# Performance work log

Hardware: AMD Instinct MI355X
Metric: run time of the kernel (lower is better)

## Reference

```python
import jax, jax.numpy as jnp
import numpy as np

DIM = 1024
HID = 512
N_EXPERTS = 16
TOP_K = 4


def setup_inputs() -> dict:
    key = jax.random.key(0)
    ks = jax.random.split(key, 8)
    s = 0.02
    x = jax.random.normal(ks[0], (2, 1024, DIM), dtype=jnp.float32)
    gate_w = jax.random.normal(ks[1], (N_EXPERTS, DIM), dtype=jnp.float32) * s
    # stacked expert weights (nn.Linear stores [out, in]; we keep [E, out, in])
    w1 = jax.random.normal(ks[2], (N_EXPERTS, HID, DIM), dtype=jnp.float32) * s
    w3 = jax.random.normal(ks[3], (N_EXPERTS, HID, DIM), dtype=jnp.float32) * s
    w2 = jax.random.normal(ks[4], (N_EXPERTS, DIM, HID), dtype=jnp.float32) * s
    sw1 = jax.random.normal(ks[5], (HID, DIM), dtype=jnp.float32) * s
    sw3 = jax.random.normal(ks[6], (HID, DIM), dtype=jnp.float32) * s
    sw2 = jax.random.normal(ks[7], (DIM, HID), dtype=jnp.float32) * s
    return {"x": x, "gate_w": gate_w, "w1": w1, "w3": w3, "w2": w2,
            "sw1": sw1, "sw3": sw3, "sw2": sw2}


def reference(x, gate_w, w1, w3, w2, sw1, sw3, sw2):
    bsz, seq_len, dim = x.shape
    xf = x.reshape(-1, dim)                              # [T, d]
    T = xf.shape[0]

    # router: softmax -> top-k -> renormalize
    probs = jax.nn.softmax(xf @ gate_w.T, axis=-1)       # [T, E]
    top_w, top_idx = jax.lax.top_k(probs, TOP_K)         # [T, K]
    top_w = top_w / jnp.sum(top_w, axis=-1, keepdims=True)

    # combine weights as dense [T, E] (zero for unselected experts);
    # weighted dense per-expert compute is mathematically identical to the
    # gather/scatter loop since unselected experts get weight 0.
    rows = jnp.arange(T)[:, None]
    combine = jnp.zeros((T, N_EXPERTS), dtype=xf.dtype).at[rows, top_idx].set(top_w)

    h1 = jnp.einsum('td,ehd->teh', xf, w1)               # [T, E, h]
    h3 = jnp.einsum('td,ehd->teh', xf, w3)
    act = jax.nn.silu(h1) * h3
    eout = jnp.einsum('teh,edh->ted', act, w2)           # [T, E, d]
    moe_out = jnp.einsum('ted,te->td', eout, combine)    # [T, d]

    shared = (jax.nn.silu(xf @ sw1.T) * (xf @ sw3.T)) @ sw2.T
    return (moe_out + shared).reshape(bsz, seq_len, dim)
```

## Files before the change

kernel.cpp:

```cpp
#include <hip/hip_runtime.h>

#define DIM   1024
#define HID   512
#define NEXP  16
#define TOPK  4
#define SLOTS 5
#define PITCH 72
#define TPE   16

typedef unsigned short u16;
typedef unsigned int   u32;
typedef short bf16x8 __attribute__((ext_vector_type(8)));
typedef float f32x4  __attribute__((ext_vector_type(4)));

__device__ __forceinline__ float bf2f(u16 u) {
    union { u32 i; float f; } v; v.i = ((u32)u) << 16; return v.f;
}
__device__ __forceinline__ u16 f2bf(float f) {
    union { float f; u32 i; } v; v.f = f;
    u32 lsb = (v.i >> 16) & 1u;
    v.i += 0x7fffu + lsb;
    return (u16)(v.i >> 16);
}
__device__ __forceinline__ uint4 pack8(float4 a, float4 b) {
    uint4 r;
    r.x = (u32)f2bf(a.x) | ((u32)f2bf(a.y) << 16);
    r.y = (u32)f2bf(a.z) | ((u32)f2bf(a.w) << 16);
    r.z = (u32)f2bf(b.x) | ((u32)f2bf(b.y) << 16);
    r.w = (u32)f2bf(b.z) | ((u32)f2bf(b.w) << 16);
    return r;
}

#define CW ((size_t)NEXP * HID * DIM / 8)
#define CS ((size_t)HID * DIM / 8)
#define SEG_B0 (CW)
#define SEG_B1 (SEG_B0 + CS)
#define SEG_B2 (SEG_B1 + CW)
#define SEG_B3 (SEG_B2 + CS)
#define SEG_B4 (SEG_B3 + CW)
#define SEG_B5 (SEG_B4 + CS)

__global__ __launch_bounds__(256) void moe_prep(
    const float* __restrict__ x,    const float* __restrict__ gate,
    const float* __restrict__ w1,   const float* __restrict__ w3,
    const float* __restrict__ w2,   const float* __restrict__ sw1,
    const float* __restrict__ sw3,  const float* __restrict__ sw2,
    u16* __restrict__ dst,
    int* __restrict__ counts, u32* __restrict__ pairs,
    float* __restrict__ wslot, int T)
{
    const int blk = blockIdx.x;
    const int tid = threadIdx.x;
    if (blk >= T) {
        const size_t base = (size_t)(blk - T) * 512 + tid;
        const size_t totC = SEG_B5 + ((size_t)T << 7);
#pragma unroll
        for (int h = 0; h < 2; ++h) {
            const size_t c = base + (size_t)h * 256;
            if (c >= totC) break;
            const float* src; size_t loc;
            if      (c < SEG_B0) { src = w1;  loc = c; }
            else if (c < SEG_B1) { src = sw1; loc = c - SEG_B0; }
            else if (c < SEG_B2) { src = w3;  loc = c - SEG_B1; }
            else if (c < SEG_B3) { src = sw3; loc = c - SEG_B2; }
            else if (c < SEG_B4) { src = w2;  loc = c - SEG_B3; }
            else if (c < SEG_B5) { src = sw2; loc = c - SEG_B4; }
            else                 { src = x;   loc = c - SEG_B5; }
            float4 a = ((const float4*)src)[loc * 2];
            float4 b = ((const float4*)src)[loc * 2 + 1];
            ((uint4*)dst)[c] = pack8(a, b);
        }
        return;
    }
    const int t    = blk;
    const int lane = tid & 63;
    const int wv   = tid >> 6;
    const float* xrow = x + (size_t)t * DIM;
    float xr[16];
#pragma unroll
    for (int j = 0; j < 16; ++j) xr[j] = xrow[lane + 64 * j];

    __shared__ float slog[NEXP];
#pragma unroll
    for (int i = 0; i < 4; ++i) {
        const int e = wv * 4 + i;
        const float* g = gate + (size_t)e * DIM;
        float s = 0.f;
#pragma unroll
        for (int j = 0; j < 16; ++j) s += xr[j] * g[lane + 64 * j];
#pragma unroll
        for (int off = 32; off > 0; off >>= 1) s += __shfl_xor(s, off);
        if (lane == 0) slog[e] = s;
    }
    __syncthreads();
    if (wv != 0) return;

    float v[NEXP];
#pragma unroll
    for (int e = 0; e < NEXP; ++e) v[e] = slog[e];
    int idx[TOPK]; float lv[TOPK];
#pragma unroll
    for (int r = 0; r < TOPK; ++r) {
        int be = 0; float bv = v[0];
        for (int e = 1; e < NEXP; ++e) { if (v[e] > bv) { bv = v[e]; be = e; } }
        idx[r] = be; lv[r] = bv; v[be] = -3.0e38f;
    }
    float wk[TOPK]; float wsum = 0.f;
#pragma unroll
    for (int r = 0; r < TOPK; ++r) { wk[r] = __expf(lv[r] - lv[0]); wsum += wk[r]; }
#pragma unroll
    for (int r = 0; r < TOPK; ++r) wk[r] /= wsum;

    if (lane < TOPK) {
        int e = idx[lane];
        int slot = atomicAdd(&counts[e], 1);
        if (slot < T) pairs[(size_t)e * T + slot] = ((u32)t << 3) | (u32)lane;
        wslot[t * SLOTS + lane] = wk[lane];
    } else if (lane == TOPK) {
        pairs[(size_t)NEXP * T + t] = ((u32)t << 3) | 4u;
        wslot[t * SLOTS + 4] = 1.0f;
    }
}

__global__ __launch_bounds__(256) void moe_gemm1(
    const u16* __restrict__ xb,
    const u16* __restrict__ w1c, const u16* __restrict__ w3c,
    const u32* __restrict__ pairs, const int* __restrict__ counts,
    u16* __restrict__ act, int T)
{
    const int e   = blockIdx.y >> 4;
    const int r0  = (blockIdx.y & (TPE - 1)) << 7;
    const int cnt = (e == NEXP) ? T : min(max(counts[e], 0), T);
    if (r0 >= cnt) return;
    const int nv = min(128, cnt - r0);
    const int n0 = blockIdx.x * 64;

    const u16* W1 = w1c + (size_t)e * HID * DIM;
    const u16* W3 = w3c + (size_t)e * HID * DIM;

    __shared__ __align__(16) u16 sA [128 * PITCH];
    __shared__ __align__(16) u16 sB1[ 64 * PITCH];
    __shared__ __align__(16) u16 sB3[ 64 * PITCH];
    __shared__ u32 sEnt[128];

    const int tid = threadIdx.x;
    if (tid < 128) {
        u32 ent = (tid < nv) ? pairs[(size_t)e * T + r0 + tid] : 0u;
        u32 tk = ent >> 3, sl = ent & 7u;
        if (tk >= (u32)T) tk = 0;
        if (sl >= SLOTS)  sl = 0;
        sEnt[tid] = (tk << 3) | sl;
    }
    __syncthreads();

    const int ar = tid >> 1;
    const int ac = (tid & 1) * 32;
    const u16* xrow = xb + (size_t)(sEnt[ar] >> 3) * DIM;
    const int br = tid >> 2;
    const int bc = (tid & 3) * 16;
    const u16* b1row = W1 + (size_t)(n0 + br) * DIM;
    const u16* b3row = W3 + (size_t)(n0 + br) * DIM;

    const int wv   = tid >> 6;
    const int lane = tid & 63;
    const int l15  = lane & 15;
    const int kq   = (lane >> 4) * 8;
    const int m0   = wv * 32;

    f32x4 acc1[2][4], acc3[2][4];
#pragma unroll
    for (int i = 0; i < 2; ++i)
#pragma unroll
        for (int j = 0; j < 4; ++j) { acc1[i][j] = (f32x4){0,0,0,0}; acc3[i][j] = (f32x4){0,0,0,0}; }

    for (int kt = 0; kt < DIM; kt += 64) {
        __syncthreads();
        *(uint4*)&sA [ar*PITCH + ac]      = *(const uint4*)&xrow [kt + ac];
        *(uint4*)&sA [ar*PITCH + ac +  8] = *(const uint4*)&xrow [kt + ac +  8];
        *(uint4*)&sA [ar*PITCH + ac + 16] = *(const uint4*)&xrow [kt + ac + 16];
        *(uint4*)&sA [ar*PITCH + ac + 24] = *(const uint4*)&xrow [kt + ac + 24];
        *(uint4*)&sB1[br*PITCH + bc]      = *(const uint4*)&b1row[kt + bc];
        *(uint4*)&sB1[br*PITCH + bc +  8] = *(const uint4*)&b1row[kt + bc + 8];
        *(uint4*)&sB3[br*PITCH + bc]      = *(const uint4*)&b3row[kt + bc];
        *(uint4*)&sB3[br*PITCH + bc +  8] = *(const uint4*)&b3row[kt + bc + 8];
        __syncthreads();
#pragma unroll
        for (int ks = 0; ks < 64; ks += 32) {
            bf16x8 a0 = *(const bf16x8*)&sA[(m0      + l15)*PITCH + ks + kq];
            bf16x8 a1 = *(const bf16x8*)&sA[(m0 + 16 + l15)*PITCH + ks + kq];
#pragma unroll
            for (int nt = 0; nt < 4; ++nt) {
                bf16x8 b1 = *(const bf16x8*)&sB1[(nt*16 + l15)*PITCH + ks + kq];
                bf16x8 b3 = *(const bf16x8*)&sB3[(nt*16 + l15)*PITCH + ks + kq];
                acc1[0][nt] = __builtin_amdgcn_mfma_f32_16x16x32_bf16(a0, b1, acc1[0][nt], 0, 0, 0);
                acc1[1][nt] = __builtin_amdgcn_mfma_f32_16x16x32_bf16(a1, b1, acc1[1][nt], 0, 0, 0);
                acc3[0][nt] = __builtin_amdgcn_mfma_f32_16x16x32_bf16(a0, b3, acc3[0][nt], 0, 0, 0);
                acc3[1][nt] = __builtin_amdgcn_mfma_f32_16x16x32_bf16(a1, b3, acc3[1][nt], 0, 0, 0);
            }
        }
    }
#pragma unroll
    for (int mf = 0; mf < 2; ++mf)
#pragma unroll
    for (int nt = 0; nt < 4; ++nt)
#pragma unroll
    for (int r = 0; r < 4; ++r) {
        int ml = m0 + mf*16 + (lane >> 4)*4 + r;
        if (ml < nv) {
            float h1 = acc1[mf][nt][r], h3 = acc3[mf][nt][r];
            float a = (h1 / (1.f + __expf(-h1))) * h3;
            u32 ent = sEnt[ml];
            size_t sidx = (size_t)(ent >> 3) * SLOTS + (ent & 7u);
            act[sidx * HID + n0 + nt*16 + l15] = f2bf(a);
        }
    }
}

__global__ __launch_bounds__(256) void moe_gemm2(
    const u16* __restrict__ act, const u16* __restrict__ w2c,
    const u32* __restrict__ pairs, const float* __restrict__ wslot,
    const int* __restrict__ counts,
    u16* __restrict__ eout, float* __restrict__ out, int useEout, int T)
{
    const int e   = blockIdx.y >> 4;
    const int r0  = (blockIdx.y & (TPE - 1)) << 7;
    const int cnt = (e == NEXP) ? T : min(max(counts[e], 0), T);
    if (r0 >= cnt) return;
    const int nv = min(128, cnt - r0);
    const int n0 = blockIdx.x * 128;

    const u16* W2 = w2c + (size_t)e * DIM * HID;

    __shared__ __align__(16) u16 sA[128 * PITCH];
    __shared__ __align__(16) u16 sB[128 * PITCH];
    __shared__ u32 sEnt[128];

    const int tid = threadIdx.x;
    if (tid < 128) {
        u32 ent = (tid < nv) ? pairs[(size_t)e * T + r0 + tid] : 0u;
        u32 tk = ent >> 3, sl = ent & 7u;
        if (tk >= (u32)T) tk = 0;
        if (sl >= SLOTS)  sl = 0;
        sEnt[tid] = (tk << 3) | sl;
    }
    __syncthreads();

    const int ar = tid >> 1;
    const int ac = (tid & 1) * 32;
    const u32 entA = sEnt[ar];
    const u16* arow = act + ((size_t)(entA >> 3) * SLOTS + (entA & 7u)) * HID;
    const u16* brow = W2 + (size_t)(n0 + ar) * HID;

    const int wv   = tid >> 6;
    const int lane = tid & 63;
    const int l15  = lane & 15;
    const int kq   = (lane >> 4) * 8;
    const int m0   = (wv & 1) * 64;
    const int nc0  = (wv >> 1) * 64;

    f32x4 acc[4][4];
#pragma unroll
    for (int i = 0; i < 4; ++i)
#pragma unroll
        for (int j = 0; j < 4; ++j) acc[i][j] = (f32x4){0,0,0,0};

    for (int kt = 0; kt < HID; kt += 64) {
        __syncthreads();
        *(uint4*)&sA[ar*PITCH + ac]      = *(const uint4*)&arow[kt + ac];
        *(uint4*)&sA[ar*PITCH + ac +  8] = *(const uint4*)&arow[kt + ac +  8];
        *(uint4*)&sA[ar*PITCH + ac + 16] = *(const uint4*)&arow[kt + ac + 16];
        *(uint4*)&sA[ar*PITCH + ac + 24] = *(const uint4*)&arow[kt + ac + 24];
        *(uint4*)&sB[ar*PITCH + ac]      = *(const uint4*)&brow[kt + ac];
        *(uint4*)&sB[ar*PITCH + ac +  8] = *(const uint4*)&brow[kt + ac +  8];
        *(uint4*)&sB[ar*PITCH + ac + 16] = *(const uint4*)&brow[kt + ac + 16];
        *(uint4*)&sB[ar*PITCH + ac + 24] = *(const uint4*)&brow[kt + ac + 24];
        __syncthreads();
#pragma unroll
        for (int ks = 0; ks < 64; ks += 32) {
            bf16x8 af[4], bf[4];
#pragma unroll
            for (int mf = 0; mf < 4; ++mf)
                af[mf] = *(const bf16x8*)&sA[(m0 + mf*16 + l15)*PITCH + ks + kq];
#pragma unroll
            for (int nf = 0; nf < 4; ++nf)
                bf[nf] = *(const bf16x8*)&sB[(nc0 + nf*16 + l15)*PITCH + ks + kq];
#pragma unroll
            for (int mf = 0; mf < 4; ++mf)
#pragma unroll
                for (int nf = 0; nf < 4; ++nf)
                    acc[mf][nf] = __builtin_amdgcn_mfma_f32_16x16x32_bf16(af[mf], bf[nf], acc[mf][nf], 0, 0, 0);
        }
    }
#pragma unroll
    for (int mf = 0; mf < 4; ++mf)
#pragma unroll
    for (int nf = 0; nf < 4; ++nf)
#pragma unroll
    for (int r = 0; r < 4; ++r) {
        int ml = m0 + mf*16 + (lane >> 4)*4 + r;
        if (ml < nv) {
            u32 ent = sEnt[ml];
            u32 tk = ent >> 3;
            float cw = wslot[tk * SLOTS + (ent & 7u)];
            int col = n0 + nc0 + nf*16 + l15;
            float v = cw * acc[mf][nf][r];
            if (useEout) {
                size_t sidx = (size_t)tk * SLOTS + (ent & 7u);
                eout[sidx * DIM + col] = f2bf(v);
            } else {
                atomicAdd(&out[(size_t)tk * DIM + col], v);
            }
        }
    }
}

__global__ __launch_bounds__(256) void moe_combine(
    const u16* __restrict__ eout, float* __restrict__ out, int n4)
{
    int i = blockIdx.x * 256 + threadIdx.x;
    if (i >= n4) return;
    int o4 = i * 4;
    int t = o4 >> 10;
    int col = o4 & 1023;
    float a0 = 0.f, a1 = 0.f, a2 = 0.f, a3 = 0.f;
#pragma unroll
    for (int s = 0; s < SLOTS; ++s) {
        const u16* row = eout + ((size_t)t * SLOTS + s) * DIM + col;
        ushort4 u = *(const ushort4*)row;
        a0 += bf2f(u.x); a1 += bf2f(u.y); a2 += bf2f(u.z); a3 += bf2f(u.w);
    }
    float4* op = (float4*)(out + (size_t)t * DIM + col);
    *op = (float4){a0, a1, a2, a3};
}

extern "C" void kernel_launch(void* const* d_in, const int* in_sizes, int n_in,
                              void* d_out, int out_size, void* d_ws, size_t ws_size,
                              hipStream_t stream)
{
    (void)n_in; (void)out_size;
    const float* x    = (const float*)d_in[0];
    const float* gate = (const float*)d_in[1];
    const float* w1   = (const float*)d_in[2];
    const float* w3   = (const float*)d_in[3];
    const float* w2   = (const float*)d_in[4];
    const float* sw1  = (const float*)d_in[5];
    const float* sw3  = (const float*)d_in[6];
    const float* sw2  = (const float*)d_in[7];
    float* out = (float*)d_out;
    const int T = in_sizes[0] / DIM;

    char* w = (char*)d_ws;
    int*  counts = (int*)(w);
    size_t off = 4096;
    u32*   pairs = (u32*)(w + off);  off += (size_t)(NEXP + 1) * T * 4;
    float* wslot = (float*)(w + off); off += (size_t)T * SLOTS * 4;
    off = (off + 255) & ~(size_t)255;
    u16*   actb  = (u16*)(w + off);  off += (size_t)T * SLOTS * HID * 2;
    off = (off + 255) & ~(size_t)255;
    u16*   cvtb  = (u16*)(w + off);
    const size_t xChunks = (size_t)T * DIM / 8;
    const size_t cvtChunks = SEG_B5 + xChunks;
    off += cvtChunks * 8 * 2;
    off = (off + 255) & ~(size_t)255;
    u16*   eoutb = (u16*)(w + off);
    const size_t needEout = off + (size_t)T * SLOTS * DIM * 2;

    u16* W1c = cvtb;
    u16* W3c = cvtb + SEG_B1 * 8;
    u16* W2c = cvtb + SEG_B3 * 8;
    u16* xb  = cvtb + SEG_B5 * 8;

    const int useEout = (ws_size >= needEout) ? 1 : 0;

    hipMemsetAsync(w, 0, 256, stream);
    if (!useEout)
        hipMemsetAsync(out, 0, (size_t)T * DIM * sizeof(float), stream);

    const int nCvt = (int)((cvtChunks + 511) / 512);
    moe_prep<<<T + nCvt, 256, 0, stream>>>(
        x, gate, w1, w3, w2, sw1, sw3, sw2, cvtb, counts, pairs, wslot, T);

    moe_gemm1<<<dim3(HID / 64, (NEXP + 1) * TPE), 256, 0, stream>>>(
        xb, W1c, W3c, pairs, counts, actb, T);
    moe_gemm2<<<dim3(DIM / 128, (NEXP + 1) * TPE), 256, 0, stream>>>(
        actb, W2c, pairs, wslot, counts, eoutb, out, useEout, T);
    if (useEout)
        moe_combine<<<(T * DIM / 4 + 255) / 256, 256, 0, stream>>>(
            eoutb, out, T * DIM / 4);
}
```

Baseline: 266.9 us.

## Fuse fp32-to-bf16 conversion into GEMM tile loads and swizzle block order

Removes the separate bulk conversion pass that turned all expert weights and x into bf16 in a workspace. The GEMM kernels now read fp32 weights and activations directly and pack them to bf16 while staging tiles into shared memory. The grids become 1D with a block-index swizzle so that blocks sharing a weight tile or row tile run close together. In exchange each GEMM tile load moves twice the bytes from global memory, and weight tiles reused by several row tiles get converted more than once.

New measurement: 381.5 us. +43.0%, slower.

```diff
diff --git a/kernel.cpp b/kernel.cpp
--- a/kernel.cpp
+++ b/kernel.cpp
@@ -31,48 +31,13 @@
     return r;
 }
 
-#define CW ((size_t)NEXP * HID * DIM / 8)
-#define CS ((size_t)HID * DIM / 8)
-#define SEG_B0 (CW)
-#define SEG_B1 (SEG_B0 + CS)
-#define SEG_B2 (SEG_B1 + CW)
-#define SEG_B3 (SEG_B2 + CS)
-#define SEG_B4 (SEG_B3 + CW)
-#define SEG_B5 (SEG_B4 + CS)
-
-__global__ __launch_bounds__(256) void moe_prep(
-    const float* __restrict__ x,    const float* __restrict__ gate,
-    const float* __restrict__ w1,   const float* __restrict__ w3,
-    const float* __restrict__ w2,   const float* __restrict__ sw1,
-    const float* __restrict__ sw3,  const float* __restrict__ sw2,
-    u16* __restrict__ dst,
+__global__ __launch_bounds__(256) void moe_router(
+    const float* __restrict__ x, const float* __restrict__ gate,
     int* __restrict__ counts, u32* __restrict__ pairs,
     float* __restrict__ wslot, int T)
 {
-    const int blk = blockIdx.x;
-    const int tid = threadIdx.x;
-    if (blk >= T) {
-        const size_t base = (size_t)(blk - T) * 512 + tid;
-        const size_t totC = SEG_B5 + ((size_t)T << 7);
-#pragma unroll
-        for (int h = 0; h < 2; ++h) {
-            const size_t c = base + (size_t)h * 256;
-            if (c >= totC) break;
-            const float* src; size_t loc;
-            if      (c < SEG_B0) { src = w1;  loc = c; }
-            else if (c < SEG_B1) { src = sw1; loc = c - SEG_B0; }
-            else if (c < SEG_B2) { src = w3;  loc = c - SEG_B1; }
-            else if (c < SEG_B3) { src = sw3; loc = c - SEG_B2; }
-            else if (c < SEG_B4) { src = w2;  loc = c - SEG_B3; }
-            else if (c < SEG_B5) { src = sw2; loc = c - SEG_B4; }
-            else                 { src = x;   loc = c - SEG_B5; }
-            float4 a = ((const float4*)src)[loc * 2];
-            float4 b = ((const float4*)src)[loc * 2 + 1];
-            ((uint4*)dst)[c] = pack8(a, b);
-        }
-        return;
-    }
-    const int t    = blk;
+    const int t    = blockIdx.x;
+    const int tid  = threadIdx.x;
     const int lane = tid & 63;
     const int wv   = tid >> 6;
     const float* xrow = x + (size_t)t * DIM;
@@ -122,21 +87,26 @@
     }
 }
 
+#define NB1 ((HID / 64) * (NEXP + 1) * TPE)
 __global__ __launch_bounds__(256) void moe_gemm1(
-    const u16* __restrict__ xb,
-    const u16* __restrict__ w1c, const u16* __restrict__ w3c,
+    const float* __restrict__ x,
+    const float* __restrict__ w1,  const float* __restrict__ w3,
+    const float* __restrict__ sw1, const float* __restrict__ sw3,
     const u32* __restrict__ pairs, const int* __restrict__ counts,
     u16* __restrict__ act, int T)
 {
-    const int e   = blockIdx.y >> 4;
-    const int r0  = (blockIdx.y & (TPE - 1)) << 7;
+    const int lin = blockIdx.x;
+    const int swz = (lin & 7) * (NB1 / 8) + (lin >> 3);
+    const int ytile = swz >> 3;
+    const int n0    = (swz & 7) * 64;
+    const int e   = ytile >> 4;
+    const int r0  = (ytile & (TPE - 1)) << 7;
     const int cnt = (e == NEXP) ? T : min(max(counts[e], 0), T);
     if (r0 >= cnt) return;
     const int nv = min(128, cnt - r0);
-    const int n0 = blockIdx.x * 64;
-
-    const u16* W1 = w1c + (size_t)e * HID * DIM;
-    const u16* W3 = w3c + (size_t)e * HID * DIM;
+
+    const float* W1 = (e == NEXP) ? sw1 : w1 + (size_t)e * HID * DIM;
+    const float* W3 = (e == NEXP) ? sw3 : w3 + (size_t)e * HID * DIM;
 
     __shared__ __align__(16) u16 sA [128 * PITCH];
     __shared__ __align__(16) u16 sB1[ 64 * PITCH];
@@ -155,11 +125,11 @@
 
     const int ar = tid >> 1;
     const int ac = (tid & 1) * 32;
-    const u16* xrow = xb + (size_t)(sEnt[ar] >> 3) * DIM;
+    const float* xrow = x + (size_t)(sEnt[ar] >> 3) * DIM;
     const int br = tid >> 2;
     const int bc = (tid & 3) * 16;
-    const u16* b1row = W1 + (size_t)(n0 + br) * DIM;
-    const u16* b3row = W3 + (size_t)(n0 + br) * DIM;
+    const float* b1row = W1 + (size_t)(n0 + br) * DIM;
+    const float* b3row = W3 + (size_t)(n0 + br) * DIM;
 
     const int wv   = tid >> 6;
     const int lane = tid & 63;
@@ -175,14 +145,23 @@
 
     for (int kt = 0; kt < DIM; kt += 64) {
         __syncthreads();
-        *(uint4*)&sA [ar*PITCH + ac]      = *(const uint4*)&xrow [kt + ac];
-        *(uint4*)&sA [ar*PITCH + ac +  8] = *(const uint4*)&xrow [kt + ac +  8];
-        *(uint4*)&sA [ar*PITCH + ac + 16] = *(const uint4*)&xrow [kt + ac + 16];
-        *(uint4*)&sA [ar*PITCH + ac + 24] = *(const uint4*)&xrow [kt + ac + 24];
-        *(uint4*)&sB1[br*PITCH + bc]      = *(const uint4*)&b1row[kt + bc];
-        *(uint4*)&sB1[br*PITCH + bc +  8] = *(const uint4*)&b1row[kt + bc + 8];
-        *(uint4*)&sB3[br*PITCH + bc]      = *(const uint4*)&b3row[kt + bc];
-        *(uint4*)&sB3[br*PITCH + bc +  8] = *(const uint4*)&b3row[kt + bc + 8];
+        {
+            const float4* ap = (const float4*)(xrow + kt + ac);
+            float4 a0 = ap[0], a1 = ap[1], a2 = ap[2], a3 = ap[3];
+            float4 a4 = ap[4], a5 = ap[5], a6 = ap[6], a7 = ap[7];
+            const float4* q1 = (const float4*)(b1row + kt + bc);
+            float4 q0 = q1[0], q1v = q1[1], q2 = q1[2], q3 = q1[3];
+            const float4* p3 = (const float4*)(b3row + kt + bc);
+            float4 r0v = p3[0], r1v = p3[1], r2v = p3[2], r3v = p3[3];
+            *(uint4*)&sA [ar*PITCH + ac]      = pack8(a0, a1);
+            *(uint4*)&sA [ar*PITCH + ac +  8] = pack8(a2, a3);
+            *(uint4*)&sA [ar*PITCH + ac + 16] = pack8(a4, a5);
+            *(uint4*)&sA [ar*PITCH + ac + 24] = pack8(a6, a7);
+            *(uint4*)&sB1[br*PITCH + bc]      = pack8(q0, q1v);
+            *(uint4*)&sB1[br*PITCH + bc +  8] = pack8(q2, q3);
+            *(uint4*)&sB3[br*PITCH + bc]      = pack8(r0v, r1v);
+            *(uint4*)&sB3[br*PITCH + bc +  8] = pack8(r2v, r3v);
+        }
         __syncthreads();
 #pragma unroll
         for (int ks = 0; ks < 64; ks += 32) {
@@ -216,20 +195,25 @@
     }
 }
 
+#define NB2 ((DIM / 128) * (NEXP + 1) * TPE)
 __global__ __launch_bounds__(256) void moe_gemm2(
-    const u16* __restrict__ act, const u16* __restrict__ w2c,
+    const u16* __restrict__ act,
+    const float* __restrict__ w2, const float* __restrict__ sw2,
     const u32* __restrict__ pairs, const float* __restrict__ wslot,
     const int* __restrict__ counts,
     u16* __restrict__ eout, float* __restrict__ out, int useEout, int T)
 {
-    const int e   = blockIdx.y >> 4;
-    const int r0  = (blockIdx.y & (TPE - 1)) << 7;
+    const int lin = blockIdx.x;
+    const int swz = (lin & 7) * (NB2 / 8) + (lin >> 3);
+    const int ytile = swz >> 3;
+    const int n0    = (swz & 7) * 128;
+    const int e   = ytile >> 4;
+    const int r0  = (ytile & (TPE - 1)) << 7;
     const int cnt = (e == NEXP) ? T : min(max(counts[e], 0), T);
     if (r0 >= cnt) return;
     const int nv = min(128, cnt - r0);
-    const int n0 = blockIdx.x * 128;
-
-    const u16* W2 = w2c + (size_t)e * DIM * HID;
+
+    const float* W2 = (e == NEXP) ? sw2 : w2 + (size_t)e * DIM * HID;
 
     __shared__ __align__(16) u16 sA[128 * PITCH];
     __shared__ __align__(16) u16 sB[128 * PITCH];
@@ -248,8 +232,8 @@
     const int ar = tid >> 1;
     const int ac = (tid & 1) * 32;
     const u32 entA = sEnt[ar];
-    const u16* arow = act + ((size_t)(entA >> 3) * SLOTS + (entA & 7u)) * HID;
-    const u16* brow = W2 + (size_t)(n0 + ar) * HID;
+    const u16*  arow = act + ((size_t)(entA >> 3) * SLOTS + (entA & 7u)) * HID;
+    const float* brow = W2 + (size_t)(n0 + ar) * HID;
 
     const int wv   = tid >> 6;
     const int lane = tid & 63;
@@ -266,14 +250,19 @@
 
     for (int kt = 0; kt < HID; kt += 64) {
         __syncthreads();
-        *(uint4*)&sA[ar*PITCH + ac]      = *(const uint4*)&arow[kt + ac];
-        *(uint4*)&sA[ar*PITCH + ac +  8] = *(const uint4*)&arow[kt + ac +  8];
-        *(uint4*)&sA[ar*PITCH + ac + 16] = *(const uint4*)&arow[kt + ac + 16];
-        *(uint4*)&sA[ar*PITCH + ac + 24] = *(const uint4*)&arow[kt + ac + 24];
-        *(uint4*)&sB[ar*PITCH + ac]      = *(const uint4*)&brow[kt + ac];
-        *(uint4*)&sB[ar*PITCH + ac +  8] = *(const uint4*)&brow[kt + ac +  8];
-        *(uint4*)&sB[ar*PITCH + ac + 16] = *(const uint4*)&brow[kt + ac + 16];
-        *(uint4*)&sB[ar*PITCH + ac + 24] = *(const uint4*)&brow[kt + ac + 24];
+        {
+            *(uint4*)&sA[ar*PITCH + ac]      = *(const uint4*)&arow[kt + ac];
+            *(uint4*)&sA[ar*PITCH + ac +  8] = *(const uint4*)&arow[kt + ac +  8];
+            *(uint4*)&sA[ar*PITCH + ac + 16] = *(const uint4*)&arow[kt + ac + 16];
+            *(uint4*)&sA[ar*PITCH + ac + 24] = *(const uint4*)&arow[kt + ac + 24];
+            const float4* bp = (const float4*)(brow + kt + ac);
+            float4 b0 = bp[0], b1 = bp[1], b2 = bp[2], b3 = bp[3];
+            float4 b4 = bp[4], b5 = bp[5], b6 = bp[6], b7 = bp[7];
+            *(uint4*)&sB[ar*PITCH + ac]      = pack8(b0, b1);
+            *(uint4*)&sB[ar*PITCH + ac +  8] = pack8(b2, b3);
+            *(uint4*)&sB[ar*PITCH + ac + 16] = pack8(b4, b5);
+            *(uint4*)&sB[ar*PITCH + ac + 24] = pack8(b6, b7);
+        }
         __syncthreads();
 #pragma unroll
         for (int ks = 0; ks < 64; ks += 32) {
@@ -357,18 +346,8 @@
     off = (off + 255) & ~(size_t)255;
     u16*   actb  = (u16*)(w + off);  off += (size_t)T * SLOTS * HID * 2;
     off = (off + 255) & ~(size_t)255;
-    u16*   cvtb  = (u16*)(w + off);
-    const size_t xChunks = (size_t)T * DIM / 8;
-    const size_t cvtChunks = SEG_B5 + xChunks;
-    off += cvtChunks * 8 * 2;
-    off = (off + 255) & ~(size_t)255;
     u16*   eoutb = (u16*)(w + off);
     const size_t needEout = off + (size_t)T * SLOTS * DIM * 2;
-
-    u16* W1c = cvtb;
-    u16* W3c = cvtb + SEG_B1 * 8;
-    u16* W2c = cvtb + SEG_B3 * 8;
-    u16* xb  = cvtb + SEG_B5 * 8;
 
     const int useEout = (ws_size >= needEout) ? 1 : 0;
 
@@ -376,14 +355,12 @@
     if (!useEout)
         hipMemsetAsync(out, 0, (size_t)T * DIM * sizeof(float), stream);
 
-    const int nCvt = (int)((cvtChunks + 511) / 512);
-    moe_prep<<<T + nCvt, 256, 0, stream>>>(
-        x, gate, w1, w3, w2, sw1, sw3, sw2, cvtb, counts, pairs, wslot, T);
-
-    moe_gemm1<<<dim3(HID / 64, (NEXP + 1) * TPE), 256, 0, stream>>>(
-        xb, W1c, W3c, pairs, counts, actb, T);
-    moe_gemm2<<<dim3(DIM / 128, (NEXP + 1) * TPE), 256, 0, stream>>>(
-        actb, W2c, pairs, wslot, counts, eoutb, out, useEout, T);
+    moe_router<<<T, 256, 0, stream>>>(x, gate, counts, pairs, wslot, T);
+
+    moe_gemm1<<<NB1, 256, 0, stream>>>(
+        x, w1, w3, sw1, sw3, pairs, counts, actb, T);
+    moe_gemm2<<<NB2, 256, 0, stream>>>(
+        actb, w2, sw2, pairs, wslot, counts, eoutb, out, useEout, T);
     if (useEout)
         moe_combine<<<(T * DIM / 4 + 255) / 256, 256, 0, stream>>>(
             eoutb, out, T * DIM / 4);
```

## Enlarge GEMM tiles: 128x128 dual-B tile in gemm1, 256x128 tile in gemm2

Applied to the files above, without the earlier changes.

The gate/up GEMM now computes a 128-token by 128-hidden tile per block, with each wave holding a 64x64 sub-tile for both W1 and W3. The down-projection GEMM now covers 256 rows by 128 output columns, and each wave computes a 64x128 sub-tile. Larger tiles raise MFMA work per LDS fragment load and cut redundant global loads of weights and activations. The cost is more accumulator registers (acc1/acc3 at 4x4 each, acc at 4x8) and more LDS per block, so occupancy may drop, and there are fewer blocks to spread across CUs.

Result: slower. 403.3 us (+51.1%).

```diff
diff --git a/kernel.cpp b/kernel.cpp
--- a/kernel.cpp
+++ b/kernel.cpp
@@ -7,6 +7,7 @@
 #define SLOTS 5
 #define PITCH 72
 #define TPE   16
+#define TPE2  8
 
 typedef unsigned short u16;
 typedef unsigned int   u32;
@@ -128,19 +129,20 @@
     const u32* __restrict__ pairs, const int* __restrict__ counts,
     u16* __restrict__ act, int T)
 {
-    const int e   = blockIdx.y >> 4;
-    const int r0  = (blockIdx.y & (TPE - 1)) << 7;
+    const int ytile = blockIdx.y;
+    const int n0    = blockIdx.x * 128;
+    const int e   = ytile >> 4;
+    const int r0  = (ytile & (TPE - 1)) << 7;
     const int cnt = (e == NEXP) ? T : min(max(counts[e], 0), T);
     if (r0 >= cnt) return;
     const int nv = min(128, cnt - r0);
-    const int n0 = blockIdx.x * 64;
 
     const u16* W1 = w1c + (size_t)e * HID * DIM;
     const u16* W3 = w3c + (size_t)e * HID * DIM;
 
     __shared__ __align__(16) u16 sA [128 * PITCH];
-    __shared__ __align__(16) u16 sB1[ 64 * PITCH];
-    __shared__ __align__(16) u16 sB3[ 64 * PITCH];
+    __shared__ __align__(16) u16 sB1[128 * PITCH];
+    __shared__ __align__(16) u16 sB3[128 * PITCH];
     __shared__ u32 sEnt[128];
 
     const int tid = threadIdx.x;
@@ -155,21 +157,20 @@
 
     const int ar = tid >> 1;
     const int ac = (tid & 1) * 32;
-    const u16* xrow = xb + (size_t)(sEnt[ar] >> 3) * DIM;
-    const int br = tid >> 2;
-    const int bc = (tid & 3) * 16;
-    const u16* b1row = W1 + (size_t)(n0 + br) * DIM;
-    const u16* b3row = W3 + (size_t)(n0 + br) * DIM;
+    const u16* xrow  = xb + (size_t)(sEnt[ar] >> 3) * DIM;
+    const u16* b1row = W1 + (size_t)(n0 + ar) * DIM;
+    const u16* b3row = W3 + (size_t)(n0 + ar) * DIM;
 
     const int wv   = tid >> 6;
     const int lane = tid & 63;
     const int l15  = lane & 15;
     const int kq   = (lane >> 4) * 8;
-    const int m0   = wv * 32;
-
-    f32x4 acc1[2][4], acc3[2][4];
-#pragma unroll
-    for (int i = 0; i < 2; ++i)
+    const int m0   = (wv & 1) * 64;
+    const int nc0  = (wv >> 1) * 64;
+
+    f32x4 acc1[4][4], acc3[4][4];
+#pragma unroll
+    for (int i = 0; i < 4; ++i)
 #pragma unroll
         for (int j = 0; j < 4; ++j) { acc1[i][j] = (f32x4){0,0,0,0}; acc3[i][j] = (f32x4){0,0,0,0}; }
 
@@ -179,39 +180,48 @@
         *(uint4*)&sA [ar*PITCH + ac +  8] = *(const uint4*)&xrow [kt + ac +  8];
         *(uint4*)&sA [ar*PITCH + ac + 16] = *(const uint4*)&xrow [kt + ac + 16];
         *(uint4*)&sA [ar*PITCH + ac + 24] = *(const uint4*)&xrow [kt + ac + 24];
-        *(uint4*)&sB1[br*PITCH + bc]      = *(const uint4*)&b1row[kt + bc];
-        *(uint4*)&sB1[br*PITCH + bc +  8] = *(const uint4*)&b1row[kt + bc + 8];
-        *(uint4*)&sB3[br*PITCH + bc]      = *(const uint4*)&b3row[kt + bc];
-        *(uint4*)&sB3[br*PITCH + bc +  8] = *(const uint4*)&b3row[kt + bc + 8];
+        *(uint4*)&sB1[ar*PITCH + ac]      = *(const uint4*)&b1row[kt + ac];
+        *(uint4*)&sB1[ar*PITCH + ac +  8] = *(const uint4*)&b1row[kt + ac +  8];
+        *(uint4*)&sB1[ar*PITCH + ac + 16] = *(const uint4*)&b1row[kt + ac + 16];
+        *(uint4*)&sB1[ar*PITCH + ac + 24] = *(const uint4*)&b1row[kt + ac + 24];
+        *(uint4*)&sB3[ar*PITCH + ac]      = *(const uint4*)&b3row[kt + ac];
+        *(uint4*)&sB3[ar*PITCH + ac +  8] = *(const uint4*)&b3row[kt + ac +  8];
+        *(uint4*)&sB3[ar*PITCH + ac + 16] = *(const uint4*)&b3row[kt + ac + 16];
+        *(uint4*)&sB3[ar*PITCH + ac + 24] = *(const uint4*)&b3row[kt + ac + 24];
         __syncthreads();
 #pragma unroll
         for (int ks = 0; ks < 64; ks += 32) {
-            bf16x8 a0 = *(const bf16x8*)&sA[(m0      + l15)*PITCH + ks + kq];
-            bf16x8 a1 = *(const bf16x8*)&sA[(m0 + 16 + l15)*PITCH + ks + kq];
-#pragma unroll
-            for (int nt = 0; nt < 4; ++nt) {
-                bf16x8 b1 = *(const bf16x8*)&sB1[(nt*16 + l15)*PITCH + ks + kq];
-                bf16x8 b3 = *(const bf16x8*)&sB3[(nt*16 + l15)*PITCH + ks + kq];
-                acc1[0][nt] = __builtin_amdgcn_mfma_f32_16x16x32_bf16(a0, b1, acc1[0][nt], 0, 0, 0);
-                acc1[1][nt] = __builtin_amdgcn_mfma_f32_16x16x32_bf16(a1, b1, acc1[1][nt], 0, 0, 0);
-                acc3[0][nt] = __builtin_amdgcn_mfma_f32_16x16x32_bf16(a0, b3, acc3[0][nt], 0, 0, 0);
-                acc3[1][nt] = __builtin_amdgcn_mfma_f32_16x16x32_bf16(a1, b3, acc3[1][nt], 0, 0, 0);
+            bf16x8 af[4], b1f[4], b3f[4];
+#pragma unroll
+            for (int mf = 0; mf < 4; ++mf)
+                af[mf] = *(const bf16x8*)&sA[(m0 + mf*16 + l15)*PITCH + ks + kq];
+#pragma unroll
+            for (int nf = 0; nf < 4; ++nf) {
+                b1f[nf] = *(const bf16x8*)&sB1[(nc0 + nf*16 + l15)*PITCH + ks + kq];
+                b3f[nf] = *(const bf16x8*)&sB3[(nc0 + nf*16 + l15)*PITCH + ks + kq];
             }
+#pragma unroll
+            for (int mf = 0; mf < 4; ++mf)
+#pragma unroll
+                for (int nf = 0; nf < 4; ++nf) {
+                    acc1[mf][nf] = __builtin_amdgcn_mfma_f32_16x16x32_bf16(af[mf], b1f[nf], acc1[mf][nf], 0, 0, 0);
+                    acc3[mf][nf] = __builtin_amdgcn_mfma_f32_16x16x32_bf16(af[mf], b3f[nf], acc3[mf][nf], 0, 0, 0);
+                }
         }
     }
 #pragma unroll
-    for (int mf = 0; mf < 2; ++mf)
-#pragma unroll
-    for (int nt = 0; nt < 4; ++nt)
+    for (int mf = 0; mf < 4; ++mf)
+#pragma unroll
+    for (int nf = 0; nf < 4; ++nf)
 #pragma unroll
     for (int r = 0; r < 4; ++r) {
         int ml = m0 + mf*16 + (lane >> 4)*4 + r;
         if (ml < nv) {
-            float h1 = acc1[mf][nt][r], h3 = acc3[mf][nt][r];
+            float h1 = acc1[mf][nf][r], h3 = acc3[mf][nf][r];
             float a = (h1 / (1.f + __expf(-h1))) * h3;
             u32 ent = sEnt[ml];
             size_t sidx = (size_t)(ent >> 3) * SLOTS + (ent & 7u);
-            act[sidx * HID + n0 + nt*16 + l15] = f2bf(a);
+            act[sidx * HID + n0 + nc0 + nf*16 + l15] = f2bf(a);
         }
     }
 }
@@ -222,21 +232,22 @@
     const int* __restrict__ counts,
     u16* __restrict__ eout, float* __restrict__ out, int useEout, int T)
 {
-    const int e   = blockIdx.y >> 4;
-    const int r0  = (blockIdx.y & (TPE - 1)) << 7;
+    const int ytile = blockIdx.y;
+    const int n0    = blockIdx.x * 128;
+    const int e   = ytile >> 3;
+    const int r0  = (ytile & (TPE2 - 1)) << 8;
     const int cnt = (e == NEXP) ? T : min(max(counts[e], 0), T);
     if (r0 >= cnt) return;
-    const int nv = min(128, cnt - r0);
-    const int n0 = blockIdx.x * 128;
+    const int nv = min(256, cnt - r0);
 
     const u16* W2 = w2c + (size_t)e * DIM * HID;
 
-    __shared__ __align__(16) u16 sA[128 * PITCH];
+    __shared__ __align__(16) u16 sA[256 * PITCH];
     __shared__ __align__(16) u16 sB[128 * PITCH];
-    __shared__ u32 sEnt[128];
+    __shared__ u32 sEnt[256];
 
     const int tid = threadIdx.x;
-    if (tid < 128) {
+    {
         u32 ent = (tid < nv) ? pairs[(size_t)e * T + r0 + tid] : 0u;
         u32 tk = ent >> 3, sl = ent & 7u;
         if (tk >= (u32)T) tk = 0;
@@ -247,62 +258,67 @@
 
     const int ar = tid >> 1;
     const int ac = (tid & 1) * 32;
-    const u32 entA = sEnt[ar];
-    const u16* arow = act + ((size_t)(entA >> 3) * SLOTS + (entA & 7u)) * HID;
-    const u16* brow = W2 + (size_t)(n0 + ar) * HID;
+    const u32 entA0 = sEnt[ar];
+    const u32 entA1 = sEnt[ar + 128];
+    const u16* arow0 = act + ((size_t)(entA0 >> 3) * SLOTS + (entA0 & 7u)) * HID;
+    const u16* arow1 = act + ((size_t)(entA1 >> 3) * SLOTS + (entA1 & 7u)) * HID;
+    const u16* brow  = W2 + (size_t)(n0 + ar) * HID;
 
     const int wv   = tid >> 6;
     const int lane = tid & 63;
     const int l15  = lane & 15;
     const int kq   = (lane >> 4) * 8;
-    const int m0   = (wv & 1) * 64;
-    const int nc0  = (wv >> 1) * 64;
-
-    f32x4 acc[4][4];
+    const int m0w  = wv * 64;
+
+    f32x4 acc[4][8];
 #pragma unroll
     for (int i = 0; i < 4; ++i)
 #pragma unroll
-        for (int j = 0; j < 4; ++j) acc[i][j] = (f32x4){0,0,0,0};
+        for (int j = 0; j < 8; ++j) acc[i][j] = (f32x4){0,0,0,0};
 
     for (int kt = 0; kt < HID; kt += 64) {
         __syncthreads();
-        *(uint4*)&sA[ar*PITCH + ac]      = *(const uint4*)&arow[kt + ac];
-        *(uint4*)&sA[ar*PITCH + ac +  8] = *(const uint4*)&arow[kt + ac +  8];
-        *(uint4*)&sA[ar*PITCH + ac + 16] = *(const uint4*)&arow[kt + ac + 16];
-        *(uint4*)&sA[ar*PITCH + ac + 24] = *(const uint4*)&arow[kt + ac + 24];
-        *(uint4*)&sB[ar*PITCH + ac]      = *(const uint4*)&brow[kt + ac];
-        *(uint4*)&sB[ar*PITCH + ac +  8] = *(const uint4*)&brow[kt + ac +  8];
-        *(uint4*)&sB[ar*PITCH + ac + 16] = *(const uint4*)&brow[kt + ac + 16];
-        *(uint4*)&sB[ar*PITCH + ac + 24] = *(const uint4*)&brow[kt + ac + 24];
+        *(uint4*)&sA[ ar       *PITCH + ac]      = *(const uint4*)&arow0[kt + ac];
+        *(uint4*)&sA[ ar       *PITCH + ac +  8] = *(const uint4*)&arow0[kt + ac +  8];
+        *(uint4*)&sA[ ar       *PITCH + ac + 16] = *(const uint4*)&arow0[kt + ac + 16];
+        *(uint4*)&sA[ ar       *PITCH + ac + 24] = *(const uint4*)&arow0[kt + ac + 24];
+        *(uint4*)&sA[(ar + 128)*PITCH + ac]      = *(const uint4*)&arow1[kt + ac];
+        *(uint4*)&sA[(ar + 128)*PITCH + ac +  8] = *(const uint4*)&arow1[kt + ac +  8];
+        *(uint4*)&sA[(ar + 128)*PITCH + ac + 16] = *(const uint4*)&arow1[kt + ac + 16];
+        *(uint4*)&sA[(ar + 128)*PITCH + ac + 24] = *(const uint4*)&arow1[kt + ac + 24];
+        *(uint4*)&sB[ ar       *PITCH + ac]      = *(const uint4*)&brow [kt + ac];
+        *(uint4*)&sB[ ar       *PITCH + ac +  8] = *(const uint4*)&brow [kt + ac +  8];
+        *(uint4*)&sB[ ar       *PITCH + ac + 16] = *(const uint4*)&brow [kt + ac + 16];
+        *(uint4*)&sB[ ar       *PITCH + ac + 24] = *(const uint4*)&brow [kt + ac + 24];
         __syncthreads();
 #pragma unroll
         for (int ks = 0; ks < 64; ks += 32) {
-            bf16x8 af[4], bf[4];
+            bf16x8 af[4], bf[8];
 #pragma unroll
             for (int mf = 0; mf < 4; ++mf)
-                af[mf] = *(const bf16x8*)&sA[(m0 + mf*16 + l15)*PITCH + ks + kq];
-#pragma unroll
-            for (int nf = 0; nf < 4; ++nf)
-                bf[nf] = *(const bf16x8*)&sB[(nc0 + nf*16 + l15)*PITCH + ks + kq];
+                af[mf] = *(const bf16x8*)&sA[(m0w + mf*16 + l15)*PITCH + ks + kq];
+#pragma unroll
+            for (int nf = 0; nf < 8; ++nf)
+                bf[nf] = *(const bf16x8*)&sB[(nf*16 + l15)*PITCH + ks + kq];
 #pragma unroll
             for (int mf = 0; mf < 4; ++mf)
 #pragma unroll
-                for (int nf = 0; nf < 4; ++nf)
+                for (int nf = 0; nf < 8; ++nf)
                     acc[mf][nf] = __builtin_amdgcn_mfma_f32_16x16x32_bf16(af[mf], bf[nf], acc[mf][nf], 0, 0, 0);
         }
     }
 #pragma unroll
     for (int mf = 0; mf < 4; ++mf)
 #pragma unroll
-    for (int nf = 0; nf < 4; ++nf)
+    for (int nf = 0; nf < 8; ++nf)
 #pragma unroll
     for (int r = 0; r < 4; ++r) {
-        int ml = m0 + mf*16 + (lane >> 4)*4 + r;
+        int ml = m0w + mf*16 + (lane >> 4)*4 + r;
         if (ml < nv) {
             u32 ent = sEnt[ml];
             u32 tk = ent >> 3;
             float cw = wslot[tk * SLOTS + (ent & 7u)];
-            int col = n0 + nc0 + nf*16 + l15;
+            int col = n0 + nf*16 + l15;
             float v = cw * acc[mf][nf][r];
             if (useEout) {
                 size_t sidx = (size_t)tk * SLOTS + (ent & 7u);
@@ -380,9 +396,9 @@
     moe_prep<<<T + nCvt, 256, 0, stream>>>(
         x, gate, w1, w3, w2, sw1, sw3, sw2, cvtb, counts, pairs, wslot, T);
 
-    moe_gemm1<<<dim3(HID / 64, (NEXP + 1) * TPE), 256, 0, stream>>>(
+    moe_gemm1<<<dim3(HID / 128, (NEXP + 1) * TPE), 256, 0, stream>>>(
         xb, W1c, W3c, pairs, counts, actb, T);
-    moe_gemm2<<<dim3(DIM / 128, (NEXP + 1) * TPE), 256, 0, stream>>>(
+    moe_gemm2<<<dim3(DIM / 128, (NEXP + 1) * TPE2), 256, 0, stream>>>(
         actb, W2c, pairs, wslot, counts, eoutb, out, useEout, T);
     if (useEout)
         moe_combine<<<(T * DIM / 4 + 255) / 256, 256, 0, stream>>>(
```
